# Kernel tuning notes

Measured on AMD Instinct MI355X. Metric: run time of the kernel, lower is better.

The kernel has to match this reference:

```python
import jax, jax.numpy as jnp
import numpy as np

EPS = 1e-5
DEG = 2  # polynomial degree of each resgconv layer (adj powers 0..DEG-1)


def _bn(x):
    # repo's functional batchnorm(x, axis=1): standardize over the node axis per event
    m = x.mean(axis=1, keepdims=True)
    s = x.std(axis=1, keepdims=True)
    return (x - m) / (s + EPS)


def _adj(phi, eta):
    # Gaussian kernel of squared euclidean distance in the (eta, phi) plane
    d2 = (phi[:, :, None] - phi[:, None, :]) ** 2 + (eta[:, :, None] - eta[:, None, :]) ** 2
    return jnp.exp(-d2)  # [B, N, N]


def _resgconv(adj, x, W, b, Wr, br):
    # x: [B, C_in, N]; spread = concat of adj^k @ x for k in 0..DEG-1 over channels
    sp = [x]
    cur = x
    for _ in range(DEG - 1):
        cur = jnp.einsum('bij,bcj->bci', adj, cur)
        sp.append(cur)
    sp = jnp.concatenate(sp, axis=1)  # [B, C_in*DEG, N]
    out = jnp.einsum('oc,bcn->bon', W, sp) + b[None, :, None]
    res = jnp.einsum('oc,bcn->bon', Wr, x) + br[None, :, None]  # residual shortcut
    return jax.nn.relu(out) + res


def setup_inputs():
    key = jax.random.key(0)
    ks = jax.random.split(key, 32)
    B, N = 16, 2048
    dims = [3, 64, 64, 64, 64]
    inp = {
        'e': jax.random.normal(ks[0], (B, N), dtype=jnp.float32),
        'phi': jax.random.normal(ks[1], (B, N), dtype=jnp.float32),
        'eta': jax.random.normal(ks[2], (B, N), dtype=jnp.float32),
    }
    for i in range(4):
        cin, cout = dims[i], dims[i + 1]
        inp[f'W{i}'] = jax.random.normal(ks[3 + 4 * i], (cout, cin * DEG)) * (1.0 / np.sqrt(cin * DEG))
        inp[f'b{i}'] = jnp.zeros((cout,), dtype=jnp.float32)
        inp[f'Wr{i}'] = jax.random.normal(ks[4 + 4 * i], (cout, cin)) * (1.0 / np.sqrt(cin))
        inp[f'br{i}'] = jnp.zeros((cout,), dtype=jnp.float32)
    inp['fcW'] = jax.random.normal(ks[30], (1, dims[-1])) * (1.0 / np.sqrt(dims[-1]))
    inp['fcb'] = jnp.zeros((1,), dtype=jnp.float32)
    return inp


def reference(e, phi, eta, W0, b0, Wr0, br0, W1, b1, Wr1, br1, W2, b2, Wr2, br2, W3, b3, Wr3, br3, fcW, fcb):
    en = _bn(e)
    adj = _adj(phi, eta)
    x = jnp.stack([en, _bn(eta), _bn(phi)], axis=1)  # [B, 3, N]
    for (W, b, Wr, br) in ((W0, b0, Wr0, br0), (W1, b1, Wr1, br1), (W2, b2, Wr2, br2), (W3, b3, Wr3, br3)):
        x = _resgconv(adj, x, W, b, Wr, br)
    pooled = x.mean(axis=2)  # [B, C]
    out = pooled @ fcW.T + fcb  # [B, 1]
    return out[:, 0]
```

## Files before the change

### kernel.cpp

```cpp
#include <hip/hip_runtime.h>
#include <hip/hip_bf16.h>

#define NN 2048
#define NB 16
#define CAT_PITCH 136
#define RSLOT_PITCH 68
#define XT_OFF 16384
#define SMEM_BYTES 147456

typedef __attribute__((ext_vector_type(8))) short short8;
typedef __attribute__((ext_vector_type(4))) float f32x4;

static __device__ __forceinline__ float bfbits2f(short s) {
  unsigned int u = ((unsigned int)(unsigned short)s) << 16;
  float f; __builtin_memcpy(&f, &u, 4); return f;
}
static __device__ __forceinline__ short f2bfbits(float f) {
  __hip_bfloat16 h = __float2bfloat16(f);
  unsigned short us; __builtin_memcpy(&us, &h, 2); return (short)us;
}
static __device__ __forceinline__ float exp2_fast(float x) {
#if __has_builtin(__builtin_amdgcn_exp2f)
  return __builtin_amdgcn_exp2f(x);
#else
  return exp2f(x);
#endif
}
static __device__ __forceinline__ unsigned pack2bf(float f0, float f1) {
  unsigned u0, u1;
  __builtin_memcpy(&u0, &f0, 4);
  __builtin_memcpy(&u1, &f1, 4);
  return __builtin_amdgcn_perm(u1 + 0x8000u, u0 + 0x8000u, 0x07060302u);
}

static __device__ __forceinline__ void gload_lds16(const void* g, void* l) {
  __builtin_amdgcn_global_load_lds(
      (const __attribute__((address_space(1))) unsigned int*)g,
      (__attribute__((address_space(3))) unsigned int*)l, 16, 0, 0);
}

__global__ __launch_bounds__(256) void bn_kernel(
    const float* __restrict__ e, const float* __restrict__ phi,
    const float* __restrict__ eta, __hip_bfloat16* __restrict__ x0) {
  const int b = blockIdx.x;
  const int c = blockIdx.y;
  const int t = threadIdx.x;
  __hip_bfloat16* out = x0 + ((size_t)b * 64 + c) * NN;
  if (c >= 3) {
    short8 z = {0, 0, 0, 0, 0, 0, 0, 0};
    for (int idx = t * 8; idx < NN; idx += 256 * 8) *(short8*)&out[idx] = z;
    return;
  }
  const float* src = (c == 0 ? e : (c == 1 ? eta : phi)) + (size_t)b * NN;
  float sum = 0.f, sq = 0.f;
  for (int idx = t * 4; idx < NN; idx += 256 * 4) {
    float4 v = *(const float4*)&src[idx];
    sum += v.x + v.y + v.z + v.w;
    sq += v.x * v.x + v.y * v.y + v.z * v.z + v.w * v.w;
  }
  __shared__ float rs[256], rq[256];
  rs[t] = sum; rq[t] = sq;
  __syncthreads();
  for (int off = 128; off > 0; off >>= 1) {
    if (t < off) { rs[t] += rs[t + off]; rq[t] += rq[t + off]; }
    __syncthreads();
  }
  const float m = rs[0] * (1.f / NN);
  const float var = fmaxf(rq[0] * (1.f / NN) - m * m, 0.f);
  const float rinv = 1.f / (sqrtf(var) + 1e-5f);
  for (int idx = t * 4; idx < NN; idx += 256 * 4) {
    float4 v = *(const float4*)&src[idx];
    out[idx + 0] = __float2bfloat16((v.x - m) * rinv);
    out[idx + 1] = __float2bfloat16((v.y - m) * rinv);
    out[idx + 2] = __float2bfloat16((v.z - m) * rinv);
    out[idx + 3] = __float2bfloat16((v.w - m) * rinv);
  }
}

__global__ __launch_bounds__(256) void prep_kernel(
    const float* __restrict__ W0, const float* __restrict__ W1,
    const float* __restrict__ W2, const float* __restrict__ W3,
    const float* __restrict__ R0, const float* __restrict__ R1,
    const float* __restrict__ R2, const float* __restrict__ R3,
    short* __restrict__ blob) {
  const int layer = blockIdx.x;
  const float* W = layer == 0 ? W0 : layer == 1 ? W1 : layer == 2 ? W2 : W3;
  const float* R = layer == 0 ? R0 : layer == 1 ? R1 : layer == 2 ? R2 : R3;
  const int CIN = layer == 0 ? 3 : 64;
  short* base = blob + layer * 24576;
  for (int f = threadIdx.x; f < 8192; f += 256) {
    int e = f & 7, lane = (f >> 3) & 63, ks = (f >> 9) & 3, os = f >> 11;
    int o = os * 16 + (lane & 15);
    int k = ks * 32 + (lane >> 4) * 8 + e;
    float v = 0.f;
    if (k < 64) { if (k < CIN) v = W[o * 2 * CIN + k]; }
    else { int c = k - 64; if (c < CIN) v = W[o * 2 * CIN + CIN + c]; }
    short hi = f2bfbits(v);
    base[f] = hi;
    base[8192 + f] = f2bfbits(v - bfbits2f(hi));
  }
  for (int f = threadIdx.x; f < 4096; f += 256) {
    int e = f & 7, lane = (f >> 3) & 63, ks = (f >> 9) & 1, os = f >> 10;
    int o = os * 16 + (lane & 15);
    int k = ks * 32 + (lane >> 4) * 8 + e;
    float v = (k < CIN) ? R[o * CIN + k] : 0.f;
    short hi = f2bfbits(v);
    base[16384 + f] = hi;
    base[20480 + f] = f2bfbits(v - bfbits2f(hi));
  }
}

static __device__ __forceinline__ void stage_chunk(
    const short* __restrict__ xb, char* smem, int wave, int lane, int tt) {
  const int par = tt & 1;
#pragma unroll
  for (int q = 0; q < 4; ++q) {
    const int s = wave * 4 + q;
    const int jgs = s >> 3;
    const int sl = s & 7;
    const int ch = sl * 8 + (lane >> 3);
    const int jc8 = (lane & 7) ^ (ch & 7);
    const short* g = xb + (size_t)ch * NN + jgs * 256 + tt * 64 + jc8 * 8;
    char* l = smem + XT_OFF + jgs * 16384 + par * 8192 + sl * 1024;
    gload_lds16(g, l);
  }
}

__global__ __launch_bounds__(1024, 4) void layer_kernel(
    const float* __restrict__ phi, const float* __restrict__ eta,
    const __hip_bfloat16* __restrict__ x, const short* __restrict__ wcat,
    const short* __restrict__ wrb, const float* __restrict__ bias,
    const float* __restrict__ brs, __hip_bfloat16* __restrict__ xo) {
  const int b = blockIdx.y;
  const int i0 = blockIdx.x * 128;
  const int tid = threadIdx.x;
  const int wave = tid >> 6;
  const int lane = tid & 63;
  const int c0 = lane & 15;
  const int hh = lane >> 4;
  const int koff = hh * 8;
  const int rh = wave & 1;
  const int jg = wave >> 1;

  __shared__ __align__(16) char smem[SMEM_BYTES];
  float* phs = (float*)smem;
  float* ehs = phs + NN;

  const float SC = 1.20112240872f;
  {
    const float* pb = phi + (size_t)b * NN;
    const float* eb = eta + (size_t)b * NN;
    for (int idx = tid; idx < NN; idx += 1024) {
      phs[idx] = pb[idx] * SC;
      ehs[idx] = eb[idx] * SC;
    }
  }
  const short* xb = (const short*)(x + (size_t)b * 64 * NN);
  stage_chunk(xb, smem, wave, lane, 0);
  __syncthreads();

  float pi_[4], ei_[4];
#pragma unroll
  for (int mt = 0; mt < 4; ++mt) {
    const int row = i0 + rh * 64 + mt * 16 + c0;
    pi_[mt] = phs[row];
    ei_[mt] = ehs[row];
  }

  f32x4 acc[4][4];
#pragma unroll
  for (int mt = 0; mt < 4; ++mt)
#pragma unroll
    for (int cs = 0; cs < 4; ++cs) acc[mt][cs] = (f32x4){0.f, 0.f, 0.f, 0.f};

  for (int t = 0; t < 4; ++t) {
    if (t < 3) stage_chunk(xb, smem, wave, lane, t + 1);
    const char* xbuf = smem + XT_OFF + jg * 16384 + (t & 1) * 8192;
    const int jbase = jg * 256 + t * 64;
#pragma unroll
    for (int kk = 0; kk < 2; ++kk) {
      const int jb = jbase + kk * 32 + koff;
      float pj[8], ej[8];
      *(float4*)&pj[0] = *(const float4*)&phs[jb];
      *(float4*)&pj[4] = *(const float4*)&phs[jb + 4];
      *(float4*)&ej[0] = *(const float4*)&ehs[jb];
      *(float4*)&ej[4] = *(const float4*)&ehs[jb + 4];
      short8 af[4];
#pragma unroll
      for (int mt = 0; mt < 4; ++mt) {
        unsigned au[4];
#pragma unroll
        for (int p = 0; p < 4; ++p) {
          float dpa = pi_[mt] - pj[2 * p],     dea = ei_[mt] - ej[2 * p];
          float dpb = pi_[mt] - pj[2 * p + 1], deb = ei_[mt] - ej[2 * p + 1];
          float fa = exp2_fast(-(dpa * dpa + dea * dea));
          float fb = exp2_fast(-(dpb * dpb + deb * deb));
          au[p] = pack2bf(fa, fb);
        }
        __builtin_memcpy(&af[mt], au, 16);
      }
      const int jc = kk * 32 + koff;
#pragma unroll
      for (int cs = 0; cs < 4; ++cs) {
        const int ch = cs * 16 + c0;
        const int boff = (ch * 128 + jc * 2) ^ ((ch & 7) << 4);
        short8 bf = *(const short8*)(xbuf + boff);
#pragma unroll
        for (int mt = 0; mt < 4; ++mt)
          acc[mt][cs] = __builtin_amdgcn_mfma_f32_16x16x32_bf16(af[mt], bf,
                                                               acc[mt][cs], 0, 0, 0);
      }
    }
    __syncthreads();
  }

  float* red = (float*)smem;
  const int slot_sz = 64 * RSLOT_PITCH;
  if (jg >= 4) {
    float* sp = red + ((jg - 4) * 2 + rh) * slot_sz;
#pragma unroll
    for (int mt = 0; mt < 4; ++mt)
#pragma unroll
      for (int cs = 0; cs < 4; ++cs)
        *(f32x4*)&sp[(cs * 16 + c0) * RSLOT_PITCH + mt * 16 + hh * 4] = acc[mt][cs];
  }
  __syncthreads();
  if (jg < 4) {
    const float* sp = red + (jg * 2 + rh) * slot_sz;
#pragma unroll
    for (int mt = 0; mt < 4; ++mt)
#pragma unroll
      for (int cs = 0; cs < 4; ++cs)
        acc[mt][cs] += *(const f32x4*)&sp[(cs * 16 + c0) * RSLOT_PITCH + mt * 16 + hh * 4];
  }
  __syncthreads();
  if (jg >= 1 && jg < 4) {
    float* sp = red + ((jg - 1) * 2 + rh) * slot_sz;
#pragma unroll
    for (int mt = 0; mt < 4; ++mt)
#pragma unroll
      for (int cs = 0; cs < 4; ++cs)
        *(f32x4*)&sp[(cs * 16 + c0) * RSLOT_PITCH + mt * 16 + hh * 4] = acc[mt][cs];
  }
  __syncthreads();
  if (jg == 0) {
#pragma unroll
    for (int k = 0; k < 3; ++k) {
      const float* sp = red + (k * 2 + rh) * slot_sz;
#pragma unroll
      for (int mt = 0; mt < 4; ++mt)
#pragma unroll
        for (int cs = 0; cs < 4; ++cs)
          acc[mt][cs] += *(const f32x4*)&sp[(cs * 16 + c0) * RSLOT_PITCH + mt * 16 + hh * 4];
    }
  }
  __syncthreads();

  short* cat = (short*)smem;
  short* out_t = (short*)(smem + 128 * CAT_PITCH * 2);
  if (jg == 0) {
#pragma unroll
    for (int mt = 0; mt < 4; ++mt)
#pragma unroll
      for (int cs = 0; cs < 4; ++cs)
#pragma unroll
        for (int r = 0; r < 4; ++r) {
          const int irow = rh * 64 + mt * 16 + hh * 4 + r;
          cat[irow * CAT_PITCH + 64 + cs * 16 + c0] = f2bfbits(acc[mt][cs][r]);
        }
  }
  {
    const int c = tid & 63, rp = tid >> 6;
    short8 v = *(const short8*)&xb[(size_t)c * NN + i0 + rp * 8];
#pragma unroll
    for (int q = 0; q < 8; ++q) cat[(rp * 8 + q) * CAT_PITCH + c] = v[q];
  }
  __syncthreads();

  {
    const int it = wave & 7;
    const int oh = wave >> 3;
    const int irl = it * 16 + c0;
    short8 bfx[4];
#pragma unroll
    for (int ks = 0; ks < 4; ++ks)
      bfx[ks] = *(const short8*)&cat[irl * CAT_PITCH + ks * 32 + koff];
#pragma unroll
    for (int osl = 0; osl < 2; ++osl) {
      const int os = oh * 2 + osl;
      f32x4 a1 = (f32x4){0.f, 0.f, 0.f, 0.f};
      f32x4 a2 = (f32x4){0.f, 0.f, 0.f, 0.f};
#pragma unroll
      for (int ks = 0; ks < 4; ++ks) {
        short8 whi = *(const short8*)&wcat[(size_t)(((os * 4 + ks) * 64) + lane) * 8];
        short8 wlo = *(const short8*)&wcat[8192 + (size_t)(((os * 4 + ks) * 64) + lane) * 8];
        a1 = __builtin_amdgcn_mfma_f32_16x16x32_bf16(whi, bfx[ks], a1, 0, 0, 0);
        a1 = __builtin_amdgcn_mfma_f32_16x16x32_bf16(wlo, bfx[ks], a1, 0, 0, 0);
      }
#pragma unroll
      for (int ks = 0; ks < 2; ++ks) {
        short8 rhi = *(const short8*)&wrb[(size_t)(((os * 2 + ks) * 64) + lane) * 8];
        short8 rlo = *(const short8*)&wrb[4096 + (size_t)(((os * 2 + ks) * 64) + lane) * 8];
        a2 = __builtin_amdgcn_mfma_f32_16x16x32_bf16(rhi, bfx[ks], a2, 0, 0, 0);
        a2 = __builtin_amdgcn_mfma_f32_16x16x32_bf16(rlo, bfx[ks], a2, 0, 0, 0);
      }
#pragma unroll
      for (int r = 0; r < 4; ++r) {
        const int o = os * 16 + hh * 4 + r;
        float v = fmaxf(a1[r] + bias[o], 0.f) + a2[r] + brs[o];
        out_t[o * CAT_PITCH + it * 16 + c0] = f2bfbits(v);
      }
    }
  }
  __syncthreads();

  {
    const int o = tid >> 4, part = tid & 15;
    short8 v = *(const short8*)&out_t[o * CAT_PITCH + part * 8];
    short* dst = (short*)xo + (size_t)b * 64 * NN + (size_t)o * NN + i0 + part * 8;
    *(short8*)dst = v;
  }
}

__global__ __launch_bounds__(256) void final_kernel(
    const __hip_bfloat16* __restrict__ x, const float* __restrict__ fcW,
    const float* __restrict__ fcb, float* __restrict__ out) {
  const int b = blockIdx.x;
  const short* xb = (const short*)(x + (size_t)b * 64 * NN);
  float acc = 0.f;
  for (int f = threadIdx.x * 8; f < 64 * NN; f += 256 * 8) {
    short8 v = *(const short8*)&xb[f];
    const float w = fcW[f >> 11];
    float ss = 0.f;
#pragma unroll
    for (int e8 = 0; e8 < 8; ++e8) ss += bfbits2f(v[e8]);
    acc += w * ss;
  }
  __shared__ float red[256];
  red[threadIdx.x] = acc;
  __syncthreads();
  for (int off = 128; off > 0; off >>= 1) {
    if ((int)threadIdx.x < off) red[threadIdx.x] += red[threadIdx.x + off];
    __syncthreads();
  }
  if (threadIdx.x == 0) out[b] = red[0] * (1.f / NN) + fcb[0];
}

extern "C" void kernel_launch(void* const* d_in, const int* in_sizes, int n_in,
                              void* d_out, int out_size, void* d_ws, size_t ws_size,
                              hipStream_t stream) {
  const float* e   = (const float*)d_in[0];
  const float* phi = (const float*)d_in[1];
  const float* eta = (const float*)d_in[2];
  const float* W[4]  = {(const float*)d_in[3],  (const float*)d_in[7],
                        (const float*)d_in[11], (const float*)d_in[15]};
  const float* bb[4] = {(const float*)d_in[4],  (const float*)d_in[8],
                        (const float*)d_in[12], (const float*)d_in[16]};
  const float* Wr[4] = {(const float*)d_in[5],  (const float*)d_in[9],
                        (const float*)d_in[13], (const float*)d_in[17]};
  const float* br[4] = {(const float*)d_in[6],  (const float*)d_in[10],
                        (const float*)d_in[14], (const float*)d_in[18]};
  const float* fcW = (const float*)d_in[19];
  const float* fcb = (const float*)d_in[20];
  float* outp = (float*)d_out;

  const size_t XSZ = (size_t)NB * 64 * NN;
  __hip_bfloat16* xA = (__hip_bfloat16*)d_ws;
  __hip_bfloat16* xB = xA + XSZ;
  short* blob = (short*)(xB + XSZ);

  dim3 bn_grid(NB, 64);
  bn_kernel<<<bn_grid, 256, 0, stream>>>(e, phi, eta, xA);
  prep_kernel<<<4, 256, 0, stream>>>(W[0], W[1], W[2], W[3],
                                     Wr[0], Wr[1], Wr[2], Wr[3], blob);

  dim3 lgrid(NN / 128, NB);
  const __hip_bfloat16* xin = xA;
  __hip_bfloat16* xout = xB;
  for (int l = 0; l < 4; ++l) {
    const short* lb = blob + l * 24576;
    layer_kernel<<<lgrid, 1024, 0, stream>>>(phi, eta, xin, lb, lb + 16384,
                                             bb[l], br[l], xout);
    const __hip_bfloat16* t = xout; xout = (__hip_bfloat16*)xin; xin = t;
  }
  final_kernel<<<NB, 256, 0, stream>>>(xA, fcW, fcb, outp);
}
```

Baseline: 247.3 us.

## Fuse all stages into one persistent kernel with grid-wide barriers

Replaces the separate bn, prep, four layer and final kernels with one persistent kernel of 256 blocks that sync through an atomic grid barrier. phi/eta are staged once into shared memory and kept across layers, and the reduction scratch moves so it no longer overwrites them. The goal is to remove six launch gaps and the repeated per-layer phi/eta loads. The risks are barrier spin overhead, a deadlock if not all 256 blocks of 1024 threads can be resident at once, and a spin timeout that silently breaks out of the wait.

```diff
diff --git a/kernel.cpp b/kernel.cpp
--- a/kernel.cpp
+++ b/kernel.cpp
@@ -4,7 +4,6 @@
 #define NN 2048
 #define NB 16
 #define CAT_PITCH 136
-#define RSLOT_PITCH 68
 #define XT_OFF 16384
 #define SMEM_BYTES 147456
 
@@ -32,83 +31,44 @@
   __builtin_memcpy(&u1, &f1, 4);
   return __builtin_amdgcn_perm(u1 + 0x8000u, u0 + 0x8000u, 0x07060302u);
 }
-
 static __device__ __forceinline__ void gload_lds16(const void* g, void* l) {
   __builtin_amdgcn_global_load_lds(
       (const __attribute__((address_space(1))) unsigned int*)g,
       (__attribute__((address_space(3))) unsigned int*)l, 16, 0, 0);
 }
 
-__global__ __launch_bounds__(256) void bn_kernel(
-    const float* __restrict__ e, const float* __restrict__ phi,
-    const float* __restrict__ eta, __hip_bfloat16* __restrict__ x0) {
-  const int b = blockIdx.x;
-  const int c = blockIdx.y;
-  const int t = threadIdx.x;
-  __hip_bfloat16* out = x0 + ((size_t)b * 64 + c) * NN;
-  if (c >= 3) {
-    short8 z = {0, 0, 0, 0, 0, 0, 0, 0};
-    for (int idx = t * 8; idx < NN; idx += 256 * 8) *(short8*)&out[idx] = z;
-    return;
-  }
-  const float* src = (c == 0 ? e : (c == 1 ? eta : phi)) + (size_t)b * NN;
-  float sum = 0.f, sq = 0.f;
-  for (int idx = t * 4; idx < NN; idx += 256 * 4) {
-    float4 v = *(const float4*)&src[idx];
-    sum += v.x + v.y + v.z + v.w;
-    sq += v.x * v.x + v.y * v.y + v.z * v.z + v.w * v.w;
-  }
-  __shared__ float rs[256], rq[256];
-  rs[t] = sum; rq[t] = sq;
+static __device__ __forceinline__ void grid_barrier(unsigned* bar, unsigned nb) {
   __syncthreads();
-  for (int off = 128; off > 0; off >>= 1) {
-    if (t < off) { rs[t] += rs[t + off]; rq[t] += rq[t + off]; }
-    __syncthreads();
-  }
-  const float m = rs[0] * (1.f / NN);
-  const float var = fmaxf(rq[0] * (1.f / NN) - m * m, 0.f);
-  const float rinv = 1.f / (sqrtf(var) + 1e-5f);
-  for (int idx = t * 4; idx < NN; idx += 256 * 4) {
-    float4 v = *(const float4*)&src[idx];
-    out[idx + 0] = __float2bfloat16((v.x - m) * rinv);
-    out[idx + 1] = __float2bfloat16((v.y - m) * rinv);
-    out[idx + 2] = __float2bfloat16((v.z - m) * rinv);
-    out[idx + 3] = __float2bfloat16((v.w - m) * rinv);
-  }
-}
-
-__global__ __launch_bounds__(256) void prep_kernel(
-    const float* __restrict__ W0, const float* __restrict__ W1,
-    const float* __restrict__ W2, const float* __restrict__ W3,
-    const float* __restrict__ R0, const float* __restrict__ R1,
-    const float* __restrict__ R2, const float* __restrict__ R3,
-    short* __restrict__ blob) {
-  const int layer = blockIdx.x;
-  const float* W = layer == 0 ? W0 : layer == 1 ? W1 : layer == 2 ? W2 : W3;
-  const float* R = layer == 0 ? R0 : layer == 1 ? R1 : layer == 2 ? R2 : R3;
-  const int CIN = layer == 0 ? 3 : 64;
-  short* base = blob + layer * 24576;
-  for (int f = threadIdx.x; f < 8192; f += 256) {
-    int e = f & 7, lane = (f >> 3) & 63, ks = (f >> 9) & 3, os = f >> 11;
-    int o = os * 16 + (lane & 15);
-    int k = ks * 32 + (lane >> 4) * 8 + e;
-    float v = 0.f;
-    if (k < 64) { if (k < CIN) v = W[o * 2 * CIN + k]; }
-    else { int c = k - 64; if (c < CIN) v = W[o * 2 * CIN + CIN + c]; }
-    short hi = f2bfbits(v);
-    base[f] = hi;
-    base[8192 + f] = f2bfbits(v - bfbits2f(hi));
-  }
-  for (int f = threadIdx.x; f < 4096; f += 256) {
-    int e = f & 7, lane = (f >> 3) & 63, ks = (f >> 9) & 1, os = f >> 10;
-    int o = os * 16 + (lane & 15);
-    int k = ks * 32 + (lane >> 4) * 8 + e;
-    float v = (k < CIN) ? R[o * CIN + k] : 0.f;
-    short hi = f2bfbits(v);
-    base[16384 + f] = hi;
-    base[20480 + f] = f2bfbits(v - bfbits2f(hi));
-  }
-}
+  if (threadIdx.x == 0) {
+    __threadfence();
+    unsigned gen = __hip_atomic_load(&bar[1], __ATOMIC_RELAXED, __HIP_MEMORY_SCOPE_AGENT);
+    unsigned arr = __hip_atomic_fetch_add(&bar[0], 1u, __ATOMIC_ACQ_REL, __HIP_MEMORY_SCOPE_AGENT);
+    if (arr == nb - 1u) {
+      __hip_atomic_store(&bar[0], 0u, __ATOMIC_RELAXED, __HIP_MEMORY_SCOPE_AGENT);
+      __hip_atomic_store(&bar[1], gen + 1u, __ATOMIC_RELEASE, __HIP_MEMORY_SCOPE_AGENT);
+    } else {
+      long cnt = 0;
+      while (__hip_atomic_load(&bar[1], __ATOMIC_ACQUIRE, __HIP_MEMORY_SCOPE_AGENT) == gen) {
+        __builtin_amdgcn_s_sleep(8);
+        if (++cnt > (1L << 22)) break;
+      }
+    }
+  }
+  __syncthreads();
+}
+
+struct Params {
+  const float *e, *phi, *eta;
+  const float *W0, *W1, *W2, *W3;
+  const float *B0, *B1, *B2, *B3;
+  const float *R0, *R1, *R2, *R3;
+  const float *Q0, *Q1, *Q2, *Q3;
+  const float *fcW, *fcb;
+  float* out;
+  short *xA, *xB;
+  short* blob;
+  unsigned* bar;
+};
 
 static __device__ __forceinline__ void stage_chunk(
     const short* __restrict__ xb, char* smem, int wave, int lane, int tt) {
@@ -126,13 +86,11 @@
   }
 }
 
-__global__ __launch_bounds__(1024, 4) void layer_kernel(
-    const float* __restrict__ phi, const float* __restrict__ eta,
-    const __hip_bfloat16* __restrict__ x, const short* __restrict__ wcat,
-    const short* __restrict__ wrb, const float* __restrict__ bias,
-    const float* __restrict__ brs, __hip_bfloat16* __restrict__ xo) {
-  const int b = blockIdx.y;
-  const int i0 = blockIdx.x * 128;
+__global__ __launch_bounds__(1024, 4) void fused_kernel(Params p) {
+  const int bid = blockIdx.x;
+  const int b = bid >> 4;
+  const int iblk = bid & 15;
+  const int i0 = iblk * 128;
   const int tid = threadIdx.x;
   const int wave = tid >> 6;
   const int lane = tid & 63;
@@ -141,6 +99,7 @@
   const int koff = hh * 8;
   const int rh = wave & 1;
   const int jg = wave >> 1;
+  const unsigned nb = gridDim.x;
 
   __shared__ __align__(16) char smem[SMEM_BYTES];
   float* phs = (float*)smem;
@@ -148,16 +107,84 @@
 
   const float SC = 1.20112240872f;
   {
-    const float* pb = phi + (size_t)b * NN;
-    const float* eb = eta + (size_t)b * NN;
+    const float* pb = p.phi + (size_t)b * NN;
+    const float* eb = p.eta + (size_t)b * NN;
     for (int idx = tid; idx < NN; idx += 1024) {
       phs[idx] = pb[idx] * SC;
       ehs[idx] = eb[idx] * SC;
     }
   }
-  const short* xb = (const short*)(x + (size_t)b * 64 * NN);
-  stage_chunk(xb, smem, wave, lane, 0);
-  __syncthreads();
+  {
+    const float* s0 = p.e + (size_t)b * NN;
+    const float* s1 = p.eta + (size_t)b * NN;
+    const float* s2 = p.phi + (size_t)b * NN;
+    float sm0 = 0.f, sq0 = 0.f, sm1 = 0.f, sq1 = 0.f, sm2 = 0.f, sq2 = 0.f;
+    for (int idx = tid; idx < NN; idx += 1024) {
+      float v0 = s0[idx], v1 = s1[idx], v2 = s2[idx];
+      sm0 += v0; sq0 += v0 * v0;
+      sm1 += v1; sq1 += v1 * v1;
+      sm2 += v2; sq2 += v2 * v2;
+    }
+    float* bscr = (float*)(smem + XT_OFF);
+    bscr[tid] = sm0; bscr[1024 + tid] = sq0;
+    bscr[2048 + tid] = sm1; bscr[3072 + tid] = sq1;
+    bscr[4096 + tid] = sm2; bscr[5120 + tid] = sq2;
+    __syncthreads();
+    for (int off = 512; off > 0; off >>= 1) {
+      if (tid < off) {
+#pragma unroll
+        for (int f = 0; f < 6; ++f)
+          bscr[f * 1024 + tid] += bscr[f * 1024 + tid + off];
+      }
+      __syncthreads();
+    }
+    float m0 = bscr[0] * (1.f / NN), m1 = bscr[2048] * (1.f / NN), m2 = bscr[4096] * (1.f / NN);
+    float r0 = 1.f / (sqrtf(fmaxf(bscr[1024] * (1.f / NN) - m0 * m0, 0.f)) + 1e-5f);
+    float r1 = 1.f / (sqrtf(fmaxf(bscr[3072] * (1.f / NN) - m1 * m1, 0.f)) + 1e-5f);
+    float r2 = 1.f / (sqrtf(fmaxf(bscr[5120] * (1.f / NN) - m2 * m2, 0.f)) + 1e-5f);
+    const int ch = tid >> 4, part = tid & 15;
+    short8 v = {0, 0, 0, 0, 0, 0, 0, 0};
+    if (ch < 3) {
+      const float* src = ch == 0 ? s0 : (ch == 1 ? s1 : s2);
+      const float mm = ch == 0 ? m0 : (ch == 1 ? m1 : m2);
+      const float rr = ch == 0 ? r0 : (ch == 1 ? r1 : r2);
+#pragma unroll
+      for (int q = 0; q < 8; ++q) v[q] = f2bfbits((src[i0 + part * 8 + q] - mm) * rr);
+    }
+    *(short8*)&p.xA[((size_t)b * 64 + ch) * NN + i0 + part * 8] = v;
+  }
+  if (bid < 4) {
+    const int l = bid;
+    const float* W = l == 0 ? p.W0 : l == 1 ? p.W1 : l == 2 ? p.W2 : p.W3;
+    const float* R = l == 0 ? p.R0 : l == 1 ? p.R1 : l == 2 ? p.R2 : p.R3;
+    const float* BI = l == 0 ? p.B0 : l == 1 ? p.B1 : l == 2 ? p.B2 : p.B3;
+    const float* QI = l == 0 ? p.Q0 : l == 1 ? p.Q1 : l == 2 ? p.Q2 : p.Q3;
+    const int CIN = l == 0 ? 3 : 64;
+    short* base = p.blob + l * 25088;
+    for (int f = tid; f < 8192; f += 1024) {
+      int e8 = f & 7, ln = (f >> 3) & 63, ks = (f >> 9) & 3, os = f >> 11;
+      int o = os * 16 + (ln & 15);
+      int k = ks * 32 + (ln >> 4) * 8 + e8;
+      float v = 0.f;
+      if (k < 64) { if (k < CIN) v = W[o * 2 * CIN + k]; }
+      else { int c = k - 64; if (c < CIN) v = W[o * 2 * CIN + CIN + c]; }
+      short hi = f2bfbits(v);
+      base[f] = hi;
+      base[8192 + f] = f2bfbits(v - bfbits2f(hi));
+    }
+    for (int f = tid; f < 4096; f += 1024) {
+      int e8 = f & 7, ln = (f >> 3) & 63, ks = (f >> 9) & 1, os = f >> 10;
+      int o = os * 16 + (ln & 15);
+      int k = ks * 32 + (ln >> 4) * 8 + e8;
+      float v = (k < CIN) ? R[o * CIN + k] : 0.f;
+      short hi = f2bfbits(v);
+      base[16384 + f] = hi;
+      base[20480 + f] = f2bfbits(v - bfbits2f(hi));
+    }
+    float* bb = (float*)((char*)base + 49152);
+    for (int f = tid; f < 64; f += 1024) { bb[f] = BI[f]; bb[64 + f] = QI[f]; }
+  }
+  grid_barrier(p.bar, nb);
 
   float pi_[4], ei_[4];
 #pragma unroll
@@ -167,221 +194,221 @@
     ei_[mt] = ehs[row];
   }
 
-  f32x4 acc[4][4];
-#pragma unroll
-  for (int mt = 0; mt < 4; ++mt)
-#pragma unroll
-    for (int cs = 0; cs < 4; ++cs) acc[mt][cs] = (f32x4){0.f, 0.f, 0.f, 0.f};
-
-  for (int t = 0; t < 4; ++t) {
-    if (t < 3) stage_chunk(xb, smem, wave, lane, t + 1);
-    const char* xbuf = smem + XT_OFF + jg * 16384 + (t & 1) * 8192;
-    const int jbase = jg * 256 + t * 64;
-#pragma unroll
-    for (int kk = 0; kk < 2; ++kk) {
-      const int jb = jbase + kk * 32 + koff;
-      float pj[8], ej[8];
-      *(float4*)&pj[0] = *(const float4*)&phs[jb];
-      *(float4*)&pj[4] = *(const float4*)&phs[jb + 4];
-      *(float4*)&ej[0] = *(const float4*)&ehs[jb];
-      *(float4*)&ej[4] = *(const float4*)&ehs[jb + 4];
-      short8 af[4];
-#pragma unroll
-      for (int mt = 0; mt < 4; ++mt) {
-        unsigned au[4];
-#pragma unroll
-        for (int p = 0; p < 4; ++p) {
-          float dpa = pi_[mt] - pj[2 * p],     dea = ei_[mt] - ej[2 * p];
-          float dpb = pi_[mt] - pj[2 * p + 1], deb = ei_[mt] - ej[2 * p + 1];
-          float fa = exp2_fast(-(dpa * dpa + dea * dea));
-          float fb = exp2_fast(-(dpb * dpb + deb * deb));
-          au[p] = pack2bf(fa, fb);
+#pragma unroll 1
+  for (int l = 0; l < 4; ++l) {
+    const short* xin = (l & 1) ? p.xB : p.xA;
+    short* xout = (l & 1) ? p.xA : p.xB;
+    const short* blobL = p.blob + l * 25088;
+    const short* wcat = blobL;
+    const short* wrb = blobL + 16384;
+    const float* bias = (const float*)((const char*)blobL + 49152);
+    const float* brs = bias + 64;
+    const short* xb = xin + (size_t)b * 64 * NN;
+
+    stage_chunk(xb, smem, wave, lane, 0);
+    __syncthreads();
+
+    f32x4 acc[4][4];
+#pragma unroll
+    for (int mt = 0; mt < 4; ++mt)
+#pragma unroll
+      for (int cs = 0; cs < 4; ++cs) acc[mt][cs] = (f32x4){0.f, 0.f, 0.f, 0.f};
+
+    for (int t = 0; t < 4; ++t) {
+      if (t < 3) stage_chunk(xb, smem, wave, lane, t + 1);
+      const char* xbuf = smem + XT_OFF + jg * 16384 + (t & 1) * 8192;
+      const int jbase = jg * 256 + t * 64;
+#pragma unroll
+      for (int kk = 0; kk < 2; ++kk) {
+        const int jb = jbase + kk * 32 + koff;
+        float pj[8], ej[8];
+        *(float4*)&pj[0] = *(const float4*)&phs[jb];
+        *(float4*)&pj[4] = *(const float4*)&phs[jb + 4];
+        *(float4*)&ej[0] = *(const float4*)&ehs[jb];
+        *(float4*)&ej[4] = *(const float4*)&ehs[jb + 4];
+        short8 af[4];
+#pragma unroll
+        for (int mt = 0; mt < 4; ++mt) {
+          unsigned au[4];
+#pragma unroll
+          for (int pp = 0; pp < 4; ++pp) {
+            float dpa = pi_[mt] - pj[2 * pp],     dea = ei_[mt] - ej[2 * pp];
+            float dpb = pi_[mt] - pj[2 * pp + 1], deb = ei_[mt] - ej[2 * pp + 1];
+            float fa = exp2_fast(-(dpa * dpa + dea * dea));
+            float fb = exp2_fast(-(dpb * dpb + deb * deb));
+            au[pp] = pack2bf(fa, fb);
+          }
+          __builtin_memcpy(&af[mt], au, 16);
         }
-        __builtin_memcpy(&af[mt], au, 16);
+        const int jc = kk * 32 + koff;
+#pragma unroll
+        for (int cs = 0; cs < 4; ++cs) {
+          const int ch = cs * 16 + c0;
+          const int boff = (ch * 128 + jc * 2) ^ ((ch & 7) << 4);
+          short8 bf = *(const short8*)(xbuf + boff);
+#pragma unroll
+          for (int mt = 0; mt < 4; ++mt)
+            acc[mt][cs] = __builtin_amdgcn_mfma_f32_16x16x32_bf16(af[mt], bf,
+                                                                 acc[mt][cs], 0, 0, 0);
+        }
       }
-      const int jc = kk * 32 + koff;
-#pragma unroll
-      for (int cs = 0; cs < 4; ++cs) {
-        const int ch = cs * 16 + c0;
-        const int boff = (ch * 128 + jc * 2) ^ ((ch & 7) << 4);
-        short8 bf = *(const short8*)(xbuf + boff);
+      __syncthreads();
+    }
+
+    char* xt = smem + XT_OFF;
+    if (jg >= 4) {
+      float* sp = (float*)(xt + ((jg - 4) * 2 + rh) * 16384);
+#pragma unroll
+      for (int mt = 0; mt < 4; ++mt)
+#pragma unroll
+        for (int cs = 0; cs < 4; ++cs)
+          *(f32x4*)&sp[((mt * 4 + cs) * 64 + lane) * 4] = acc[mt][cs];
+    }
+    __syncthreads();
+    if (jg < 4) {
+      const float* sp = (const float*)(xt + (jg * 2 + rh) * 16384);
+#pragma unroll
+      for (int mt = 0; mt < 4; ++mt)
+#pragma unroll
+        for (int cs = 0; cs < 4; ++cs)
+          acc[mt][cs] += *(const f32x4*)&sp[((mt * 4 + cs) * 64 + lane) * 4];
+    }
+    __syncthreads();
+    if (jg >= 1 && jg < 4) {
+      float* sp = (float*)(xt + ((jg - 1) * 2 + rh) * 16384);
+#pragma unroll
+      for (int mt = 0; mt < 4; ++mt)
+#pragma unroll
+        for (int cs = 0; cs < 4; ++cs)
+          *(f32x4*)&sp[((mt * 4 + cs) * 64 + lane) * 4] = acc[mt][cs];
+    }
+    __syncthreads();
+    if (jg == 0) {
+#pragma unroll
+      for (int k = 0; k < 3; ++k) {
+        const float* sp = (const float*)(xt + (k * 2 + rh) * 16384);
 #pragma unroll
         for (int mt = 0; mt < 4; ++mt)
-          acc[mt][cs] = __builtin_amdgcn_mfma_f32_16x16x32_bf16(af[mt], bf,
-                                                               acc[mt][cs], 0, 0, 0);
+#pragma unroll
+          for (int cs = 0; cs < 4; ++cs)
+            acc[mt][cs] += *(const f32x4*)&sp[((mt * 4 + cs) * 64 + lane) * 4];
       }
     }
     __syncthreads();
-  }
-
-  float* red = (float*)smem;
-  const int slot_sz = 64 * RSLOT_PITCH;
-  if (jg >= 4) {
-    float* sp = red + ((jg - 4) * 2 + rh) * slot_sz;
-#pragma unroll
-    for (int mt = 0; mt < 4; ++mt)
-#pragma unroll
-      for (int cs = 0; cs < 4; ++cs)
-        *(f32x4*)&sp[(cs * 16 + c0) * RSLOT_PITCH + mt * 16 + hh * 4] = acc[mt][cs];
-  }
-  __syncthreads();
-  if (jg < 4) {
-    const float* sp = red + (jg * 2 + rh) * slot_sz;
-#pragma unroll
-    for (int mt = 0; mt < 4; ++mt)
-#pragma unroll
-      for (int cs = 0; cs < 4; ++cs)
-        acc[mt][cs] += *(const f32x4*)&sp[(cs * 16 + c0) * RSLOT_PITCH + mt * 16 + hh * 4];
-  }
-  __syncthreads();
-  if (jg >= 1 && jg < 4) {
-    float* sp = red + ((jg - 1) * 2 + rh) * slot_sz;
-#pragma unroll
-    for (int mt = 0; mt < 4; ++mt)
-#pragma unroll
-      for (int cs = 0; cs < 4; ++cs)
-        *(f32x4*)&sp[(cs * 16 + c0) * RSLOT_PITCH + mt * 16 + hh * 4] = acc[mt][cs];
-  }
-  __syncthreads();
-  if (jg == 0) {
-#pragma unroll
-    for (int k = 0; k < 3; ++k) {
-      const float* sp = red + (k * 2 + rh) * slot_sz;
+
+    short* cat = (short*)(smem + XT_OFF);
+    short* out_t = (short*)(smem + XT_OFF + 128 * CAT_PITCH * 2);
+    if (jg == 0) {
 #pragma unroll
       for (int mt = 0; mt < 4; ++mt)
 #pragma unroll
         for (int cs = 0; cs < 4; ++cs)
-          acc[mt][cs] += *(const f32x4*)&sp[(cs * 16 + c0) * RSLOT_PITCH + mt * 16 + hh * 4];
-    }
-  }
-  __syncthreads();
-
-  short* cat = (short*)smem;
-  short* out_t = (short*)(smem + 128 * CAT_PITCH * 2);
-  if (jg == 0) {
-#pragma unroll
-    for (int mt = 0; mt < 4; ++mt)
-#pragma unroll
-      for (int cs = 0; cs < 4; ++cs)
+#pragma unroll
+          for (int r = 0; r < 4; ++r) {
+            const int irow = rh * 64 + mt * 16 + hh * 4 + r;
+            cat[irow * CAT_PITCH + 64 + cs * 16 + c0] = f2bfbits(acc[mt][cs][r]);
+          }
+    }
+    {
+      const int cch = tid & 63, rp = tid >> 6;
+      short8 v = *(const short8*)&xb[(size_t)cch * NN + i0 + rp * 8];
+#pragma unroll
+      for (int q = 0; q < 8; ++q) cat[(rp * 8 + q) * CAT_PITCH + cch] = v[q];
+    }
+    __syncthreads();
+
+    {
+      const int it = wave & 7;
+      const int oh = wave >> 3;
+      const int irl = it * 16 + c0;
+      short8 bfx[4];
+#pragma unroll
+      for (int ks = 0; ks < 4; ++ks)
+        bfx[ks] = *(const short8*)&cat[irl * CAT_PITCH + ks * 32 + koff];
+#pragma unroll
+      for (int osl = 0; osl < 2; ++osl) {
+        const int os = oh * 2 + osl;
+        f32x4 a1 = (f32x4){0.f, 0.f, 0.f, 0.f};
+        f32x4 a2 = (f32x4){0.f, 0.f, 0.f, 0.f};
+#pragma unroll
+        for (int ks = 0; ks < 4; ++ks) {
+          short8 whi = *(const short8*)&wcat[(size_t)(((os * 4 + ks) * 64) + lane) * 8];
+          short8 wlo = *(const short8*)&wcat[8192 + (size_t)(((os * 4 + ks) * 64) + lane) * 8];
+          a1 = __builtin_amdgcn_mfma_f32_16x16x32_bf16(whi, bfx[ks], a1, 0, 0, 0);
+          a1 = __builtin_amdgcn_mfma_f32_16x16x32_bf16(wlo, bfx[ks], a1, 0, 0, 0);
+        }
+#pragma unroll
+        for (int ks = 0; ks < 2; ++ks) {
+          short8 rhi = *(const short8*)&wrb[(size_t)(((os * 2 + ks) * 64) + lane) * 8];
+          short8 rlo = *(const short8*)&wrb[4096 + (size_t)(((os * 2 + ks) * 64) + lane) * 8];
+          a2 = __builtin_amdgcn_mfma_f32_16x16x32_bf16(rhi, bfx[ks], a2, 0, 0, 0);
+          a2 = __builtin_amdgcn_mfma_f32_16x16x32_bf16(rlo, bfx[ks], a2, 0, 0, 0);
+        }
 #pragma unroll
         for (int r = 0; r < 4; ++r) {
-          const int irow = rh * 64 + mt * 16 + hh * 4 + r;
-          cat[irow * CAT_PITCH + 64 + cs * 16 + c0] = f2bfbits(acc[mt][cs][r]);
+          const int o = os * 16 + hh * 4 + r;
+          float v = fmaxf(a1[r] + bias[o], 0.f) + a2[r] + brs[o];
+          out_t[o * CAT_PITCH + it * 16 + c0] = f2bfbits(v);
         }
-  }
-  {
-    const int c = tid & 63, rp = tid >> 6;
-    short8 v = *(const short8*)&xb[(size_t)c * NN + i0 + rp * 8];
-#pragma unroll
-    for (int q = 0; q < 8; ++q) cat[(rp * 8 + q) * CAT_PITCH + c] = v[q];
-  }
-  __syncthreads();
-
-  {
-    const int it = wave & 7;
-    const int oh = wave >> 3;
-    const int irl = it * 16 + c0;
-    short8 bfx[4];
-#pragma unroll
-    for (int ks = 0; ks < 4; ++ks)
-      bfx[ks] = *(const short8*)&cat[irl * CAT_PITCH + ks * 32 + koff];
-#pragma unroll
-    for (int osl = 0; osl < 2; ++osl) {
-      const int os = oh * 2 + osl;
-      f32x4 a1 = (f32x4){0.f, 0.f, 0.f, 0.f};
-      f32x4 a2 = (f32x4){0.f, 0.f, 0.f, 0.f};
-#pragma unroll
-      for (int ks = 0; ks < 4; ++ks) {
-        short8 whi = *(const short8*)&wcat[(size_t)(((os * 4 + ks) * 64) + lane) * 8];
-        short8 wlo = *(const short8*)&wcat[8192 + (size_t)(((os * 4 + ks) * 64) + lane) * 8];
-        a1 = __builtin_amdgcn_mfma_f32_16x16x32_bf16(whi, bfx[ks], a1, 0, 0, 0);
-        a1 = __builtin_amdgcn_mfma_f32_16x16x32_bf16(wlo, bfx[ks], a1, 0, 0, 0);
       }
-#pragma unroll
-      for (int ks = 0; ks < 2; ++ks) {
-        short8 rhi = *(const short8*)&wrb[(size_t)(((os * 2 + ks) * 64) + lane) * 8];
-        short8 rlo = *(const short8*)&wrb[4096 + (size_t)(((os * 2 + ks) * 64) + lane) * 8];
-        a2 = __builtin_amdgcn_mfma_f32_16x16x32_bf16(rhi, bfx[ks], a2, 0, 0, 0);
-        a2 = __builtin_amdgcn_mfma_f32_16x16x32_bf16(rlo, bfx[ks], a2, 0, 0, 0);
-      }
-#pragma unroll
-      for (int r = 0; r < 4; ++r) {
-        const int o = os * 16 + hh * 4 + r;
-        float v = fmaxf(a1[r] + bias[o], 0.f) + a2[r] + brs[o];
-        out_t[o * CAT_PITCH + it * 16 + c0] = f2bfbits(v);
-      }
-    }
-  }
-  __syncthreads();
-
-  {
-    const int o = tid >> 4, part = tid & 15;
-    short8 v = *(const short8*)&out_t[o * CAT_PITCH + part * 8];
-    short* dst = (short*)xo + (size_t)b * 64 * NN + (size_t)o * NN + i0 + part * 8;
-    *(short8*)dst = v;
-  }
-}
-
-__global__ __launch_bounds__(256) void final_kernel(
-    const __hip_bfloat16* __restrict__ x, const float* __restrict__ fcW,
-    const float* __restrict__ fcb, float* __restrict__ out) {
-  const int b = blockIdx.x;
-  const short* xb = (const short*)(x + (size_t)b * 64 * NN);
-  float acc = 0.f;
-  for (int f = threadIdx.x * 8; f < 64 * NN; f += 256 * 8) {
-    short8 v = *(const short8*)&xb[f];
-    const float w = fcW[f >> 11];
-    float ss = 0.f;
-#pragma unroll
-    for (int e8 = 0; e8 < 8; ++e8) ss += bfbits2f(v[e8]);
-    acc += w * ss;
-  }
-  __shared__ float red[256];
-  red[threadIdx.x] = acc;
-  __syncthreads();
-  for (int off = 128; off > 0; off >>= 1) {
-    if ((int)threadIdx.x < off) red[threadIdx.x] += red[threadIdx.x + off];
-    __syncthreads();
-  }
-  if (threadIdx.x == 0) out[b] = red[0] * (1.f / NN) + fcb[0];
+    }
+    __syncthreads();
+
+    {
+      const int o = tid >> 4, part = tid & 15;
+      short8 v = *(const short8*)&out_t[o * CAT_PITCH + part * 8];
+      *(short8*)&xout[(size_t)b * 64 * NN + (size_t)o * NN + i0 + part * 8] = v;
+    }
+    grid_barrier(p.bar, nb);
+  }
+
+  if (iblk == 0) {
+    const short* xb = p.xA + (size_t)b * 64 * NN;
+    float acc = 0.f;
+    for (int f = tid * 8; f < 64 * NN; f += 1024 * 8) {
+      short8 v = *(const short8*)&xb[f];
+      const float w = p.fcW[f >> 11];
+      float ss = 0.f;
+#pragma unroll
+      for (int e8 = 0; e8 < 8; ++e8) ss += bfbits2f(v[e8]);
+      acc += w * ss;
+    }
+    float* fs = (float*)(smem + XT_OFF);
+    fs[tid] = acc;
+    __syncthreads();
+    for (int off = 512; off > 0; off >>= 1) {
+      if (tid < off) fs[tid] += fs[tid + off];
+      __syncthreads();
+    }
+    if (tid == 0) p.out[b] = fs[0] * (1.f / NN) + p.fcb[0];
+  }
 }
 
 extern "C" void kernel_launch(void* const* d_in, const int* in_sizes, int n_in,
                               void* d_out, int out_size, void* d_ws, size_t ws_size,
                               hipStream_t stream) {
-  const float* e   = (const float*)d_in[0];
-  const float* phi = (const float*)d_in[1];
-  const float* eta = (const float*)d_in[2];
-  const float* W[4]  = {(const float*)d_in[3],  (const float*)d_in[7],
-                        (const float*)d_in[11], (const float*)d_in[15]};
-  const float* bb[4] = {(const float*)d_in[4],  (const float*)d_in[8],
-                        (const float*)d_in[12], (const float*)d_in[16]};
-  const float* Wr[4] = {(const float*)d_in[5],  (const float*)d_in[9],
-                        (const float*)d_in[13], (const float*)d_in[17]};
-  const float* br[4] = {(const float*)d_in[6],  (const float*)d_in[10],
-                        (const float*)d_in[14], (const float*)d_in[18]};
-  const float* fcW = (const float*)d_in[19];
-  const float* fcb = (const float*)d_in[20];
-  float* outp = (float*)d_out;
+  Params p;
+  p.e = (const float*)d_in[0];
+  p.phi = (const float*)d_in[1];
+  p.eta = (const float*)d_in[2];
+  p.W0 = (const float*)d_in[3];  p.B0 = (const float*)d_in[4];
+  p.R0 = (const float*)d_in[5];  p.Q0 = (const float*)d_in[6];
+  p.W1 = (const float*)d_in[7];  p.B1 = (const float*)d_in[8];
+  p.R1 = (const float*)d_in[9];  p.Q1 = (const float*)d_in[10];
+  p.W2 = (const float*)d_in[11]; p.B2 = (const float*)d_in[12];
+  p.R2 = (const float*)d_in[13]; p.Q2 = (const float*)d_in[14];
+  p.W3 = (const float*)d_in[15]; p.B3 = (const float*)d_in[16];
+  p.R3 = (const float*)d_in[17]; p.Q3 = (const float*)d_in[18];
+  p.fcW = (const float*)d_in[19];
+  p.fcb = (const float*)d_in[20];
+  p.out = (float*)d_out;
 
   const size_t XSZ = (size_t)NB * 64 * NN;
-  __hip_bfloat16* xA = (__hip_bfloat16*)d_ws;
-  __hip_bfloat16* xB = xA + XSZ;
-  short* blob = (short*)(xB + XSZ);
-
-  dim3 bn_grid(NB, 64);
-  bn_kernel<<<bn_grid, 256, 0, stream>>>(e, phi, eta, xA);
-  prep_kernel<<<4, 256, 0, stream>>>(W[0], W[1], W[2], W[3],
-                                     Wr[0], Wr[1], Wr[2], Wr[3], blob);
-
-  dim3 lgrid(NN / 128, NB);
-  const __hip_bfloat16* xin = xA;
-  __hip_bfloat16* xout = xB;
-  for (int l = 0; l < 4; ++l) {
-    const short* lb = blob + l * 24576;
-    layer_kernel<<<lgrid, 1024, 0, stream>>>(phi, eta, xin, lb, lb + 16384,
-                                             bb[l], br[l], xout);
-    const __hip_bfloat16* t = xout; xout = (__hip_bfloat16*)xin; xin = t;
-  }
-  final_kernel<<<NB, 256, 0, stream>>>(xA, fcW, fcb, outp);
-}
+  p.xA = (short*)d_ws;
+  p.xB = p.xA + XSZ;
+  p.blob = p.xB + XSZ;
+  p.bar = (unsigned*)((char*)d_ws + (8u << 20) + (256u << 10));
+
+  hipMemsetAsync(p.bar, 0, 256, stream);
+  fused_kernel<<<256, 1024, 0, stream>>>(p);
+}
```

New measurement: 534.6 us. +116.2%, slower.

## Per-wave private staging with vmcnt pipelining, XCD-aware block remap, fuse bn+prep

Applied to the files above, without the earlier changes.

Each wave now stages its own x chunk into a private double buffer using direct global-to-LDS loads. A manual s_waitcnt vmcnt replaces the block-wide __syncthreads inside the 8-step K loop, so waves no longer wait on each other while the exp-based adjacency computation and MFMAs run. The grid becomes 1D with a block-id remap that groups blocks of the same batch onto the same XCD for L2 locality. The reduction slots move to a lane-linear layout, and the bn and weight-prep kernels are merged into one launch. The risk is that the hand-placed waitcnt and sched_barrier ordering depends on exact load counts and could be fragile.

```diff
diff --git a/kernel.cpp b/kernel.cpp
--- a/kernel.cpp
+++ b/kernel.cpp
@@ -4,7 +4,6 @@
 #define NN 2048
 #define NB 16
 #define CAT_PITCH 136
-#define RSLOT_PITCH 68
 #define XT_OFF 16384
 #define SMEM_BYTES 147456
 
@@ -32,19 +31,52 @@
   __builtin_memcpy(&u1, &f1, 4);
   return __builtin_amdgcn_perm(u1 + 0x8000u, u0 + 0x8000u, 0x07060302u);
 }
-
 static __device__ __forceinline__ void gload_lds16(const void* g, void* l) {
   __builtin_amdgcn_global_load_lds(
       (const __attribute__((address_space(1))) unsigned int*)g,
       (__attribute__((address_space(3))) unsigned int*)l, 16, 0, 0);
 }
 
-__global__ __launch_bounds__(256) void bn_kernel(
+__global__ __launch_bounds__(256) void bnprep_kernel(
     const float* __restrict__ e, const float* __restrict__ phi,
-    const float* __restrict__ eta, __hip_bfloat16* __restrict__ x0) {
+    const float* __restrict__ eta, __hip_bfloat16* __restrict__ x0,
+    const float* __restrict__ W0, const float* __restrict__ W1,
+    const float* __restrict__ W2, const float* __restrict__ W3,
+    const float* __restrict__ R0, const float* __restrict__ R1,
+    const float* __restrict__ R2, const float* __restrict__ R3,
+    short* __restrict__ blob) {
+  const int t = threadIdx.x;
+  if (blockIdx.y == 64) {
+    const int layer = blockIdx.x;
+    if (layer >= 4) return;
+    const float* W = layer == 0 ? W0 : layer == 1 ? W1 : layer == 2 ? W2 : W3;
+    const float* R = layer == 0 ? R0 : layer == 1 ? R1 : layer == 2 ? R2 : R3;
+    const int CIN = layer == 0 ? 3 : 64;
+    short* base = blob + layer * 24576;
+    for (int f = t; f < 8192; f += 256) {
+      int e8 = f & 7, ln = (f >> 3) & 63, ks = (f >> 9) & 3, os = f >> 11;
+      int o = os * 16 + (ln & 15);
+      int k = ks * 32 + (ln >> 4) * 8 + e8;
+      float v = 0.f;
+      if (k < 64) { if (k < CIN) v = W[o * 2 * CIN + k]; }
+      else { int c = k - 64; if (c < CIN) v = W[o * 2 * CIN + CIN + c]; }
+      short hi = f2bfbits(v);
+      base[f] = hi;
+      base[8192 + f] = f2bfbits(v - bfbits2f(hi));
+    }
+    for (int f = t; f < 4096; f += 256) {
+      int e8 = f & 7, ln = (f >> 3) & 63, ks = (f >> 9) & 1, os = f >> 10;
+      int o = os * 16 + (ln & 15);
+      int k = ks * 32 + (ln >> 4) * 8 + e8;
+      float v = (k < CIN) ? R[o * CIN + k] : 0.f;
+      short hi = f2bfbits(v);
+      base[16384 + f] = hi;
+      base[20480 + f] = f2bfbits(v - bfbits2f(hi));
+    }
+    return;
+  }
   const int b = blockIdx.x;
   const int c = blockIdx.y;
-  const int t = threadIdx.x;
   __hip_bfloat16* out = x0 + ((size_t)b * 64 + c) * NN;
   if (c >= 3) {
     short8 z = {0, 0, 0, 0, 0, 0, 0, 0};
@@ -77,62 +109,15 @@
   }
 }
 
-__global__ __launch_bounds__(256) void prep_kernel(
-    const float* __restrict__ W0, const float* __restrict__ W1,
-    const float* __restrict__ W2, const float* __restrict__ W3,
-    const float* __restrict__ R0, const float* __restrict__ R1,
-    const float* __restrict__ R2, const float* __restrict__ R3,
-    short* __restrict__ blob) {
-  const int layer = blockIdx.x;
-  const float* W = layer == 0 ? W0 : layer == 1 ? W1 : layer == 2 ? W2 : W3;
-  const float* R = layer == 0 ? R0 : layer == 1 ? R1 : layer == 2 ? R2 : R3;
-  const int CIN = layer == 0 ? 3 : 64;
-  short* base = blob + layer * 24576;
-  for (int f = threadIdx.x; f < 8192; f += 256) {
-    int e = f & 7, lane = (f >> 3) & 63, ks = (f >> 9) & 3, os = f >> 11;
-    int o = os * 16 + (lane & 15);
-    int k = ks * 32 + (lane >> 4) * 8 + e;
-    float v = 0.f;
-    if (k < 64) { if (k < CIN) v = W[o * 2 * CIN + k]; }
-    else { int c = k - 64; if (c < CIN) v = W[o * 2 * CIN + CIN + c]; }
-    short hi = f2bfbits(v);
-    base[f] = hi;
-    base[8192 + f] = f2bfbits(v - bfbits2f(hi));
-  }
-  for (int f = threadIdx.x; f < 4096; f += 256) {
-    int e = f & 7, lane = (f >> 3) & 63, ks = (f >> 9) & 1, os = f >> 10;
-    int o = os * 16 + (lane & 15);
-    int k = ks * 32 + (lane >> 4) * 8 + e;
-    float v = (k < CIN) ? R[o * CIN + k] : 0.f;
-    short hi = f2bfbits(v);
-    base[16384 + f] = hi;
-    base[20480 + f] = f2bfbits(v - bfbits2f(hi));
-  }
-}
-
-static __device__ __forceinline__ void stage_chunk(
-    const short* __restrict__ xb, char* smem, int wave, int lane, int tt) {
-  const int par = tt & 1;
-#pragma unroll
-  for (int q = 0; q < 4; ++q) {
-    const int s = wave * 4 + q;
-    const int jgs = s >> 3;
-    const int sl = s & 7;
-    const int ch = sl * 8 + (lane >> 3);
-    const int jc8 = (lane & 7) ^ (ch & 7);
-    const short* g = xb + (size_t)ch * NN + jgs * 256 + tt * 64 + jc8 * 8;
-    char* l = smem + XT_OFF + jgs * 16384 + par * 8192 + sl * 1024;
-    gload_lds16(g, l);
-  }
-}
-
 __global__ __launch_bounds__(1024, 4) void layer_kernel(
     const float* __restrict__ phi, const float* __restrict__ eta,
     const __hip_bfloat16* __restrict__ x, const short* __restrict__ wcat,
     const short* __restrict__ wrb, const float* __restrict__ bias,
     const float* __restrict__ brs, __hip_bfloat16* __restrict__ xo) {
-  const int b = blockIdx.y;
-  const int i0 = blockIdx.x * 128;
+  const int bid = blockIdx.x;
+  const int sid = (bid & 7) * 32 + (bid >> 3);
+  const int b = sid >> 4;
+  const int i0 = (sid & 15) * 128;
   const int tid = threadIdx.x;
   const int wave = tid >> 6;
   const int lane = tid & 63;
@@ -156,7 +141,24 @@
     }
   }
   const short* xb = (const short*)(x + (size_t)b * 64 * NN);
-  stage_chunk(xb, smem, wave, lane, 0);
+
+  const int d4 = lane & 1, d5 = (lane >> 1) & 1, d6 = (lane >> 2) & 1;
+  const int d7 = (lane >> 3) & 1, d8 = (lane >> 4) & 1, d9 = (lane >> 5) & 1;
+  const int ch_l = (d9 << 3) | (d8 << 2) | (d7 << 1) | (d6 ^ d8);
+  const int jb8 = ((d5 ^ d7) << 1) | (d4 ^ d6 ^ d8);
+  char* wbuf = smem + XT_OFF + wave * 8192;
+
+#define STAGE(tt)                                                             \
+  {                                                                           \
+    const int _t = (tt);                                                      \
+    _Pragma("unroll")                                                         \
+    for (int gsl = 0; gsl < 4; ++gsl)                                         \
+      gload_lds16(xb + (size_t)(gsl * 16 + ch_l) * NN + jg * 256 + _t * 32 +  \
+                      jb8 * 8,                                                \
+                  wbuf + (_t & 1) * 4096 + gsl * 1024);                       \
+  }
+
+  STAGE(0);
   __syncthreads();
 
   float pi_[4], ei_[4];
@@ -173,91 +175,98 @@
 #pragma unroll
     for (int cs = 0; cs < 4; ++cs) acc[mt][cs] = (f32x4){0.f, 0.f, 0.f, 0.f};
 
-  for (int t = 0; t < 4; ++t) {
-    if (t < 3) stage_chunk(xb, smem, wave, lane, t + 1);
-    const char* xbuf = smem + XT_OFF + jg * 16384 + (t & 1) * 8192;
-    const int jbase = jg * 256 + t * 64;
-#pragma unroll
-    for (int kk = 0; kk < 2; ++kk) {
-      const int jb = jbase + kk * 32 + koff;
-      float pj[8], ej[8];
-      *(float4*)&pj[0] = *(const float4*)&phs[jb];
-      *(float4*)&pj[4] = *(const float4*)&phs[jb + 4];
-      *(float4*)&ej[0] = *(const float4*)&ehs[jb];
-      *(float4*)&ej[4] = *(const float4*)&ehs[jb + 4];
-      short8 af[4];
-#pragma unroll
-      for (int mt = 0; mt < 4; ++mt) {
-        unsigned au[4];
-#pragma unroll
-        for (int p = 0; p < 4; ++p) {
-          float dpa = pi_[mt] - pj[2 * p],     dea = ei_[mt] - ej[2 * p];
-          float dpb = pi_[mt] - pj[2 * p + 1], deb = ei_[mt] - ej[2 * p + 1];
-          float fa = exp2_fast(-(dpa * dpa + dea * dea));
-          float fb = exp2_fast(-(dpb * dpb + deb * deb));
-          au[p] = pack2bf(fa, fb);
-        }
-        __builtin_memcpy(&af[mt], au, 16);
-      }
-      const int jc = kk * 32 + koff;
-#pragma unroll
-      for (int cs = 0; cs < 4; ++cs) {
-        const int ch = cs * 16 + c0;
-        const int boff = (ch * 128 + jc * 2) ^ ((ch & 7) << 4);
-        short8 bf = *(const short8*)(xbuf + boff);
-#pragma unroll
-        for (int mt = 0; mt < 4; ++mt)
-          acc[mt][cs] = __builtin_amdgcn_mfma_f32_16x16x32_bf16(af[mt], bf,
-                                                               acc[mt][cs], 0, 0, 0);
-      }
-    }
-    __syncthreads();
-  }
-
-  float* red = (float*)smem;
-  const int slot_sz = 64 * RSLOT_PITCH;
+#define COMPUTE(tt)                                                           \
+  {                                                                           \
+    const int _t = (tt);                                                      \
+    const char* xbuf = wbuf + (_t & 1) * 4096;                                \
+    const int jb = jg * 256 + _t * 32 + koff;                                 \
+    float pj[8], ej[8];                                                       \
+    *(float4*)&pj[0] = *(const float4*)&phs[jb];                              \
+    *(float4*)&pj[4] = *(const float4*)&phs[jb + 4];                          \
+    *(float4*)&ej[0] = *(const float4*)&ehs[jb];                              \
+    *(float4*)&ej[4] = *(const float4*)&ehs[jb + 4];                          \
+    short8 af[4];                                                             \
+    _Pragma("unroll")                                                         \
+    for (int mt = 0; mt < 4; ++mt) {                                          \
+      unsigned au[4];                                                         \
+      _Pragma("unroll")                                                       \
+      for (int pp = 0; pp < 4; ++pp) {                                        \
+        float dpa = pi_[mt] - pj[2 * pp],     dea = ei_[mt] - ej[2 * pp];     \
+        float dpb = pi_[mt] - pj[2 * pp + 1], deb = ei_[mt] - ej[2 * pp + 1]; \
+        float fa = exp2_fast(-(dpa * dpa + dea * dea));                       \
+        float fb = exp2_fast(-(dpb * dpb + deb * deb));                       \
+        au[pp] = pack2bf(fa, fb);                                             \
+      }                                                                       \
+      __builtin_memcpy(&af[mt], au, 16);                                      \
+    }                                                                         \
+    _Pragma("unroll")                                                         \
+    for (int cs = 0; cs < 4; ++cs) {                                          \
+      short8 bf = *(const short8*)(xbuf + cs * 1024 +                         \
+                                   ((c0 * 64 + koff * 2) ^ ((c0 & 7) << 4))); \
+      _Pragma("unroll")                                                       \
+      for (int mt = 0; mt < 4; ++mt)                                          \
+        acc[mt][cs] = __builtin_amdgcn_mfma_f32_16x16x32_bf16(af[mt], bf,     \
+                                                          acc[mt][cs], 0, 0, 0); \
+    }                                                                         \
+  }
+
+#pragma unroll 1
+  for (int t = 0; t < 7; ++t) {
+    STAGE(t + 1);
+    __builtin_amdgcn_sched_barrier(0);
+    asm volatile("s_waitcnt vmcnt(4)" ::: "memory");
+    __builtin_amdgcn_sched_barrier(0);
+    COMPUTE(t);
+    __builtin_amdgcn_sched_barrier(0);
+  }
+  asm volatile("s_waitcnt vmcnt(0)" ::: "memory");
+  __builtin_amdgcn_sched_barrier(0);
+  COMPUTE(7);
+  __syncthreads();
+
+  char* xt = smem + XT_OFF;
   if (jg >= 4) {
-    float* sp = red + ((jg - 4) * 2 + rh) * slot_sz;
+    float* sp = (float*)(xt + ((jg - 4) * 2 + rh) * 16384);
 #pragma unroll
     for (int mt = 0; mt < 4; ++mt)
 #pragma unroll
       for (int cs = 0; cs < 4; ++cs)
-        *(f32x4*)&sp[(cs * 16 + c0) * RSLOT_PITCH + mt * 16 + hh * 4] = acc[mt][cs];
+        *(f32x4*)&sp[((mt * 4 + cs) * 64 + lane) * 4] = acc[mt][cs];
   }
   __syncthreads();
   if (jg < 4) {
-    const float* sp = red + (jg * 2 + rh) * slot_sz;
+    const float* sp = (const float*)(xt + (jg * 2 + rh) * 16384);
 #pragma unroll
     for (int mt = 0; mt < 4; ++mt)
 #pragma unroll
       for (int cs = 0; cs < 4; ++cs)
-        acc[mt][cs] += *(const f32x4*)&sp[(cs * 16 + c0) * RSLOT_PITCH + mt * 16 + hh * 4];
+        acc[mt][cs] += *(const f32x4*)&sp[((mt * 4 + cs) * 64 + lane) * 4];
   }
   __syncthreads();
   if (jg >= 1 && jg < 4) {
-    float* sp = red + ((jg - 1) * 2 + rh) * slot_sz;
+    float* sp = (float*)(xt + ((jg - 1) * 2 + rh) * 16384);
 #pragma unroll
     for (int mt = 0; mt < 4; ++mt)
 #pragma unroll
       for (int cs = 0; cs < 4; ++cs)
-        *(f32x4*)&sp[(cs * 16 + c0) * RSLOT_PITCH + mt * 16 + hh * 4] = acc[mt][cs];
+        *(f32x4*)&sp[((mt * 4 + cs) * 64 + lane) * 4] = acc[mt][cs];
   }
   __syncthreads();
   if (jg == 0) {
 #pragma unroll
     for (int k = 0; k < 3; ++k) {
-      const float* sp = red + (k * 2 + rh) * slot_sz;
+      const float* sp = (const float*)(xt + (k * 2 + rh) * 16384);
 #pragma unroll
       for (int mt = 0; mt < 4; ++mt)
 #pragma unroll
         for (int cs = 0; cs < 4; ++cs)
-          acc[mt][cs] += *(const f32x4*)&sp[(cs * 16 + c0) * RSLOT_PITCH + mt * 16 + hh * 4];
-    }
-  }
-  __syncthreads();
-
-  short* cat = (short*)smem;
-  short* out_t = (short*)(smem + 128 * CAT_PITCH * 2);
+          acc[mt][cs] += *(const f32x4*)&sp[((mt * 4 + cs) * 64 + lane) * 4];
+    }
+  }
+  __syncthreads();
+
+  short* cat = (short*)(smem + XT_OFF);
+  short* out_t = (short*)(smem + XT_OFF + 128 * CAT_PITCH * 2);
   if (jg == 0) {
 #pragma unroll
     for (int mt = 0; mt < 4; ++mt)
@@ -270,10 +279,10 @@
         }
   }
   {
-    const int c = tid & 63, rp = tid >> 6;
-    short8 v = *(const short8*)&xb[(size_t)c * NN + i0 + rp * 8];
-#pragma unroll
-    for (int q = 0; q < 8; ++q) cat[(rp * 8 + q) * CAT_PITCH + c] = v[q];
+    const int cch = tid & 63, rp = tid >> 6;
+    short8 v = *(const short8*)&xb[(size_t)cch * NN + i0 + rp * 8];
+#pragma unroll
+    for (int q = 0; q < 8; ++q) cat[(rp * 8 + q) * CAT_PITCH + cch] = v[q];
   }
   __syncthreads();
 
@@ -317,9 +326,10 @@
   {
     const int o = tid >> 4, part = tid & 15;
     short8 v = *(const short8*)&out_t[o * CAT_PITCH + part * 8];
-    short* dst = (short*)xo + (size_t)b * 64 * NN + (size_t)o * NN + i0 + part * 8;
-    *(short8*)dst = v;
-  }
+    *(short8*)((short*)xo + (size_t)b * 64 * NN + (size_t)o * NN + i0 + part * 8) = v;
+  }
+#undef STAGE
+#undef COMPUTE
 }
 
 __global__ __launch_bounds__(256) void final_kernel(
@@ -369,18 +379,15 @@
   __hip_bfloat16* xB = xA + XSZ;
   short* blob = (short*)(xB + XSZ);
 
-  dim3 bn_grid(NB, 64);
-  bn_kernel<<<bn_grid, 256, 0, stream>>>(e, phi, eta, xA);
-  prep_kernel<<<4, 256, 0, stream>>>(W[0], W[1], W[2], W[3],
-                                     Wr[0], Wr[1], Wr[2], Wr[3], blob);
-
-  dim3 lgrid(NN / 128, NB);
+  bnprep_kernel<<<dim3(16, 65), 256, 0, stream>>>(
+      e, phi, eta, xA, W[0], W[1], W[2], W[3], Wr[0], Wr[1], Wr[2], Wr[3], blob);
+
   const __hip_bfloat16* xin = xA;
   __hip_bfloat16* xout = xB;
   for (int l = 0; l < 4; ++l) {
     const short* lb = blob + l * 24576;
-    layer_kernel<<<lgrid, 1024, 0, stream>>>(phi, eta, xin, lb, lb + 16384,
-                                             bb[l], br[l], xout);
+    layer_kernel<<<256, 1024, 0, stream>>>(phi, eta, xin, lb, lb + 16384,
+                                           bb[l], br[l], xout);
     const __hip_bfloat16* t = xout; xout = (__hip_bfloat16*)xin; xin = t;
   }
   final_kernel<<<NB, 256, 0, stream>>>(xA, fcW, fcb, outp);
```

After: 237.9 us. 1.04x faster.
